# Optimization experiments

Hardware: AMD Instinct MI355X
Metric: run time of the kernel (lower is better)

## Reference

```python
import jax, jax.numpy as jnp
import numpy as np

DIM = 1024
NUM_HEADS = 16
DIM_HEAD = 64
POOL = 8  # int(sqrt(agent_num=64))
SCALE = DIM_HEAD ** -0.5


def setup_inputs() -> dict:
    key = jax.random.key(0)
    k1, k2, k3, k4 = jax.random.split(key, 4)
    inner = NUM_HEADS * DIM_HEAD
    x = jax.random.normal(k1, (4, 4096, DIM), dtype=jnp.float32)
    # qkv Linear (no bias): weight stored as (in, out) so forward is x @ Wqkv
    Wqkv = jax.random.normal(k2, (DIM, 3 * inner), dtype=jnp.float32) * (DIM ** -0.5)
    Wo = jax.random.normal(k3, (inner, DIM), dtype=jnp.float32) * (inner ** -0.5)
    bo = jax.random.normal(k4, (DIM,), dtype=jnp.float32) * 0.01
    return {"x": x, "Wqkv": Wqkv, "Wo": Wo, "bo": bo}


def reference(x, Wqkv, Wo, bo):
    b, t, _ = x.shape
    h, d = NUM_HEADS, DIM_HEAD
    qkv = x @ Wqkv                                   # [b, t, 3*h*d]
    qkv = qkv.reshape(b, t, 3, h, d)                 # split (qkv h d)
    qkv = jnp.transpose(qkv, (2, 0, 3, 1, 4))        # [3, b, h, t, d]
    q, k, v = qkv[0], qkv[1], qkv[2]
    # AdaptiveAvgPool2d((POOL, d)) on [b,h,t,d]: identity on d, mean-pool t -> POOL
    # (t divisible by POOL -> exact reshape+mean)
    agent = q.reshape(b, h, POOL, t // POOL, d).mean(axis=3)  # [b, h, P, d]
    # stage 1: agents attend over keys, aggregate values
    s1 = jnp.einsum('bhid,bhjd->bhij', agent * SCALE, k)      # [b, h, P, t]
    p1 = jax.nn.softmax(s1, axis=-1)
    v_agent = jnp.einsum('bhij,bhjd->bhid', p1, v)            # [b, h, P, d]
    # stage 2: queries attend over agent tokens
    s2 = jnp.einsum('bhid,bhjd->bhij', q * SCALE, agent)      # [b, h, t, P]
    p2 = jax.nn.softmax(s2, axis=-1)
    out = jnp.einsum('bhij,bhjd->bhid', p2, v_agent)          # [b, h, t, d]
    out = jnp.transpose(out, (0, 2, 1, 3)).reshape(b, t, h * d)
    return out @ Wo + bo
```

## Files before the change

kernel.cpp:

```cpp
#include <hip/hip_runtime.h>
#include <hip/hip_bf16.h>
#include <stdint.h>

typedef __bf16 bf16;
typedef __attribute__((ext_vector_type(8))) __bf16 bf16x8;
typedef __attribute__((ext_vector_type(2))) __bf16 bf16x2;
typedef __attribute__((ext_vector_type(4))) float f32x4;

#define NH 16
#define DH 64
#define POOL 8
#define BATCH 4
#define SEQ 4096
#define DIMV 1024
#define QKV_N (3*DIMV)
#define M_TOTAL (BATCH*SEQ)
#define SCALE_F 0.125f
#define BH (BATCH*NH)
#define QKVSZ ((size_t)BH*SEQ*DH)
#define TCH 8
#define TCL (SEQ/TCH)
#define HP 128

#define AS1(p) ((const __attribute__((address_space(1))) void*)(p))
#define AS3(p) ((__attribute__((address_space(3))) void*)(p))

__global__ void convert_x(const float* __restrict__ in, bf16* __restrict__ out) {
  size_t i = ((size_t)blockIdx.x * 256 + threadIdx.x) * 8;
  float4 f0 = *(const float4*)(in + i);
  float4 f1 = *(const float4*)(in + i + 4);
  bf16x8 o;
  o[0] = (bf16)f0.x; o[1] = (bf16)f0.y; o[2] = (bf16)f0.z; o[3] = (bf16)f0.w;
  o[4] = (bf16)f1.x; o[5] = (bf16)f1.y; o[6] = (bf16)f1.z; o[7] = (bf16)f1.w;
  *(bf16x8*)(out + i) = o;
}

__global__ void transpose_f32_bf16(const float* __restrict__ in, bf16* __restrict__ out,
                                   int R, int C) {
  __shared__ float tile[32][33];
  int c0 = blockIdx.x * 32, r0 = blockIdx.y * 32;
  int tx = threadIdx.x & 31, ty = threadIdx.x >> 5;
  for (int i = ty; i < 32; i += 8)
    tile[i][tx] = in[(size_t)(r0 + i) * C + c0 + tx];
  __syncthreads();
  for (int i = ty; i < 32; i += 8)
    out[(size_t)(c0 + i) * R + r0 + tx] = (bf16)tile[tx][i];
}

template <int MODE>
__global__ __launch_bounds__(256)
void gemm_bt(const bf16* __restrict__ A, const bf16* __restrict__ B,
             void* __restrict__ Cv, const float* __restrict__ bias,
             int M, int N, int K) {
  __shared__ bf16 As[128 * 32];
  __shared__ bf16 Bs[128 * 32];
  const int tid  = threadIdx.x;
  const int w    = tid >> 6;
  const int lane = tid & 63;
  const int m0 = blockIdx.y * 128, n0 = blockIdx.x * 128;
  const int wm = (w & 1) * 64, wn = (w >> 1) * 64;

  const bf16* Bb = (MODE == 2) ? (B + (size_t)(m0 >> 12) * N * K) : B;

  f32x4 acc[4][4] = {};

  const int g0  = w * 2;
  const int rig = lane >> 2;
  const int kcs = (lane & 3) ^ ((rig >> 1) & 3);
  const bf16* Ap0 = A + (size_t)(m0 + g0 * 16 + rig) * K + kcs * 8;
  const bf16* Ap1 = Ap0 + (size_t)16 * K;
  const bf16* Bp0 = Bb + (size_t)(n0 + g0 * 16 + rig) * K + kcs * 8;
  const bf16* Bp1 = Bp0 + (size_t)16 * K;
  bf16* AsW0 = As + g0 * 512;
  bf16* AsW1 = As + (g0 + 1) * 512;
  bf16* BsW0 = Bs + g0 * 512;
  bf16* BsW1 = Bs + (g0 + 1) * 512;

  for (int k0 = 0; k0 < K; k0 += 32) {
    __syncthreads();
    __builtin_amdgcn_global_load_lds(AS1(Ap0 + k0), AS3(AsW0), 16, 0, 0);
    __builtin_amdgcn_global_load_lds(AS1(Ap1 + k0), AS3(AsW1), 16, 0, 0);
    __builtin_amdgcn_global_load_lds(AS1(Bp0 + k0), AS3(BsW0), 16, 0, 0);
    __builtin_amdgcn_global_load_lds(AS1(Bp1 + k0), AS3(BsW1), 16, 0, 0);
    __syncthreads();

    bf16x8 a[4], b[4];
    const int C = lane >> 4;
#pragma unroll
    for (int i = 0; i < 4; ++i) {
      int ar = wm + i * 16 + (lane & 15);
      int sw = C ^ ((ar >> 1) & 3);
      a[i] = *(const bf16x8*)&As[ar * 32 + sw * 8];
    }
#pragma unroll
    for (int j = 0; j < 4; ++j) {
      int br = wn + j * 16 + (lane & 15);
      int sw = C ^ ((br >> 1) & 3);
      b[j] = *(const bf16x8*)&Bs[br * 32 + sw * 8];
    }
#pragma unroll
    for (int i = 0; i < 4; ++i)
#pragma unroll
      for (int j = 0; j < 4; ++j)
        acc[i][j] = __builtin_amdgcn_mfma_f32_16x16x32_bf16(a[i], b[j], acc[i][j], 0, 0, 0);
  }

  const int cr = (lane >> 4) * 4;
  const int cc = lane & 15;
#pragma unroll
  for (int i = 0; i < 4; ++i) {
#pragma unroll
    for (int j = 0; j < 4; ++j) {
      int rowb = m0 + wm + i * 16 + cr;
      if (MODE == 2) {
        float* Cp = (float*)Cv;
        int col = n0 + wn + j * 16 + cc;
        float bb = bias[col];
#pragma unroll
        for (int r = 0; r < 4; ++r)
          Cp[(size_t)(rowb + r) * N + col] = acc[i][j][r] + bb;
      } else {
        bf16* Cp = (bf16*)Cv;
        int nbase = n0 + wn + j * 16;
        int which = nbase >> 10;
        int hh    = (nbase >> 6) & 15;
        int dd    = (nbase & 63) + cc;
        int bb_   = rowb >> 12;
#pragma unroll
        for (int r = 0; r < 4; ++r) {
          int t = (rowb + r) & 4095;
          size_t addr = (size_t)which * QKVSZ +
                        ((size_t)(bb_ * NH + hh) * SEQ + t) * DH + dd;
          Cp[addr] = (bf16)acc[i][j][r];
        }
      }
    }
  }
}

__global__ void agent_pool(const bf16* __restrict__ q, float* __restrict__ agent) {
  int bid = blockIdx.x;
  int p = bid & 7, bh = bid >> 3;
  int d = threadIdx.x & 63, c = threadIdx.x >> 6;
  const bf16* base = q + ((size_t)bh * SEQ + p * 512) * DH + d;
  float s = 0.f;
  for (int i = c * 128; i < c * 128 + 128; ++i)
    s += (float)base[(size_t)i * DH];
  __shared__ float red[4][64];
  red[c][d] = s;
  __syncthreads();
  if (c == 0) {
    float v = (red[0][d] + red[1][d] + red[2][d] + red[3][d]) * (1.0f / 512.0f);
    agent[(size_t)(bh * POOL + p) * DH + d] = v;
  }
}

__global__ __launch_bounds__(256)
void stage1_fused(const bf16* __restrict__ k, const bf16* __restrict__ v,
                  const float* __restrict__ agent,
                  float* __restrict__ pm, float* __restrict__ pl,
                  float* __restrict__ pva) {
  const int tc = blockIdx.x, bh = blockIdx.y;
  const int tid = threadIdx.x;
  const int t0 = tc * TCL;

  __shared__ float agT[64][8];
  __shared__ float se[TCL][9];
  __shared__ float rm[4][8], rl[4][8];

  for (int i = tid; i < 512; i += 256) {
    int p = i >> 6, d = i & 63;
    agT[d][p] = agent[(size_t)bh * 512 + i] * SCALE_F;
  }
  __syncthreads();

  const bf16* kbase = k + ((size_t)bh * SEQ + t0) * DH;
  float sc[2][8] = {};
#pragma unroll
  for (int j = 0; j < 2; ++j) {
    const bf16* krow = kbase + (size_t)(j * 256 + tid) * DH;
#pragma unroll
    for (int dc = 0; dc < 8; ++dc) {
      bf16x8 k8 = *(const bf16x8*)(krow + dc * 8);
#pragma unroll
      for (int e = 0; e < 8; ++e) {
        float kv = (float)k8[e];
        int d = dc * 8 + e;
        float4 a0 = *(const float4*)&agT[d][0];
        float4 a1 = *(const float4*)&agT[d][4];
        sc[j][0] += a0.x * kv; sc[j][1] += a0.y * kv;
        sc[j][2] += a0.z * kv; sc[j][3] += a0.w * kv;
        sc[j][4] += a1.x * kv; sc[j][5] += a1.y * kv;
        sc[j][6] += a1.z * kv; sc[j][7] += a1.w * kv;
      }
    }
  }

  float mx[8];
#pragma unroll
  for (int p = 0; p < 8; ++p) mx[p] = fmaxf(sc[0][p], sc[1][p]);
#pragma unroll
  for (int o = 32; o; o >>= 1)
#pragma unroll
    for (int p = 0; p < 8; ++p) mx[p] = fmaxf(mx[p], __shfl_xor(mx[p], o));
  if ((tid & 63) == 0)
#pragma unroll
    for (int p = 0; p < 8; ++p) rm[tid >> 6][p] = mx[p];
  __syncthreads();
  float m[8];
#pragma unroll
  for (int p = 0; p < 8; ++p)
    m[p] = fmaxf(fmaxf(rm[0][p], rm[1][p]), fmaxf(rm[2][p], rm[3][p]));

  float sl[8] = {};
#pragma unroll
  for (int j = 0; j < 2; ++j) {
    int tl = j * 256 + tid;
#pragma unroll
    for (int p = 0; p < 8; ++p) {
      float e = __expf(sc[j][p] - m[p]);
      sl[p] += e;
      se[tl][p] = e;
    }
  }
#pragma unroll
  for (int o = 32; o; o >>= 1)
#pragma unroll
    for (int p = 0; p < 8; ++p) sl[p] += __shfl_xor(sl[p], o);
  if ((tid & 63) == 0)
#pragma unroll
    for (int p = 0; p < 8; ++p) rl[tid >> 6][p] = sl[p];
  __syncthreads();
  if (tid < 8) {
    float l = rl[0][tid] + rl[1][tid] + rl[2][tid] + rl[3][tid];
    pm[(size_t)(bh * TCH + tc) * 8 + tid] = m[tid];
    pl[(size_t)(bh * TCH + tc) * 8 + tid] = l;
  }

  const int p  = tid >> 5;
  const int d0 = (tid & 31) * 2;
  const bf16* vbase = v + ((size_t)bh * SEQ + t0) * DH + d0;
  float a0 = 0.f, a1 = 0.f;
#pragma unroll 8
  for (int tl = 0; tl < TCL; ++tl) {
    float wgt = se[tl][p];
    bf16x2 v2 = *(const bf16x2*)(vbase + (size_t)tl * DH);
    a0 += wgt * (float)v2[0];
    a1 += wgt * (float)v2[1];
  }
  float* o = pva + ((size_t)(bh * TCH + tc) * 8 + p) * DH + d0;
  o[0] = a0; o[1] = a1;
}

__global__ void combine_vag(const float* __restrict__ pm, const float* __restrict__ pl,
                            const float* __restrict__ pva, float* __restrict__ vag) {
  int bh = blockIdx.x;
#pragma unroll
  for (int e = threadIdx.x; e < 512; e += 256) {
    int p = e >> 6, d = e & 63;
    float M = -1e30f;
#pragma unroll
    for (int tc = 0; tc < TCH; ++tc)
      M = fmaxf(M, pm[(size_t)(bh * TCH + tc) * 8 + p]);
    float L = 0.f, acc = 0.f;
#pragma unroll
    for (int tc = 0; tc < TCH; ++tc) {
      float w = __expf(pm[(size_t)(bh * TCH + tc) * 8 + p] - M);
      L   += w * pl[(size_t)(bh * TCH + tc) * 8 + p];
      acc += w * pva[((size_t)(bh * TCH + tc) * 8 + p) * DH + d];
    }
    vag[(size_t)bh * 512 + e] = acc / L;
  }
}

__global__ void w2_build(const float* __restrict__ vag, const bf16* __restrict__ WoT,
                         bf16* __restrict__ W2T) {
  int b = blockIdx.y;
  int n = blockIdx.x * 16 + (threadIdx.x & 15);
  int h = threadIdx.x >> 4;
  __shared__ float vg[128][65];
  for (int i = threadIdx.x; i < 128 * 64; i += 256)
    vg[i >> 6][i & 63] = vag[(size_t)b * 128 * 64 + i];
  __syncthreads();
  float acc[8] = {};
  const bf16* wrow = WoT + (size_t)n * DIMV + h * 64;
#pragma unroll
  for (int dv = 0; dv < 8; ++dv) {
    bf16x8 wv = *(const bf16x8*)(wrow + dv * 8);
#pragma unroll
    for (int e = 0; e < 8; ++e) {
      float wf = (float)wv[e];
      int d = dv * 8 + e;
#pragma unroll
      for (int p = 0; p < 8; ++p) acc[p] += vg[h * 8 + p][d] * wf;
    }
  }
  bf16x8 o;
#pragma unroll
  for (int p = 0; p < 8; ++p) o[p] = (bf16)acc[p];
  *(bf16x8*)&W2T[((size_t)b * DIMV + n) * HP + h * 8] = o;
}

__global__ __launch_bounds__(256)
void p2_build(const bf16* __restrict__ q, const float* __restrict__ agent,
              bf16* __restrict__ P2) {
  const int bh = blockIdx.y;
  const int t  = blockIdx.x * 256 + threadIdx.x;
  const int tid = threadIdx.x;

  __shared__ float agT[64][8];
  for (int i = tid; i < 512; i += 256) {
    int p = i >> 6, d = i & 63;
    agT[d][p] = agent[(size_t)bh * 512 + i] * SCALE_F;
  }
  __syncthreads();

  const bf16* qrow = q + ((size_t)bh * SEQ + t) * DH;
  float sc[8] = {};
#pragma unroll
  for (int dc = 0; dc < 8; ++dc) {
    bf16x8 q8 = *(const bf16x8*)(qrow + dc * 8);
#pragma unroll
    for (int e = 0; e < 8; ++e) {
      float qv = (float)q8[e];
      int d = dc * 8 + e;
      float4 a0 = *(const float4*)&agT[d][0];
      float4 a1 = *(const float4*)&agT[d][4];
      sc[0] += a0.x * qv; sc[1] += a0.y * qv; sc[2] += a0.z * qv; sc[3] += a0.w * qv;
      sc[4] += a1.x * qv; sc[5] += a1.y * qv; sc[6] += a1.z * qv; sc[7] += a1.w * qv;
    }
  }
  float m = sc[0];
#pragma unroll
  for (int p = 1; p < 8; ++p) m = fmaxf(m, sc[p]);
  float wsum = 0.f, wgt[8];
#pragma unroll
  for (int p = 0; p < 8; ++p) { wgt[p] = __expf(sc[p] - m); wsum += wgt[p]; }
  float inv = 1.0f / wsum;
  int b = bh >> 4, h = bh & 15;
  bf16x8 o8;
#pragma unroll
  for (int p = 0; p < 8; ++p) o8[p] = (bf16)(wgt[p] * inv);
  *(bf16x8*)&P2[((size_t)(b * SEQ + t)) * HP + h * 8] = o8;
}

extern "C" void kernel_launch(void* const* d_in, const int* in_sizes, int n_in,
                              void* d_out, int out_size, void* d_ws, size_t ws_size,
                              hipStream_t stream) {
  const float* x    = (const float*)d_in[0];
  const float* Wqkv = (const float*)d_in[1];
  const float* Wo   = (const float*)d_in[2];
  const float* bo   = (const float*)d_in[3];
  float* out = (float*)d_out;

  char* ws = (char*)d_ws;
  bf16* WqkvT = (bf16*)ws;                                   ws += (size_t)QKV_N * DIMV * 2;
  bf16* WoT   = (bf16*)ws;                                   ws += (size_t)DIMV * DIMV * 2;
  bf16* qkv   = (bf16*)ws;                                   ws += 3 * QKVSZ * 2;
  char* wsu   = ws;                                          ws += (size_t)M_TOTAL * DIMV * 2;
  bf16*  xb    = (bf16*)wsu;
  bf16*  P2    = (bf16*)wsu;
  bf16*  W2T   = (bf16*)(wsu + (size_t)M_TOTAL * HP * 2);
  float* agent = (float*)ws;                                 ws += 512 * 64 * 4;
  float* pm    = (float*)ws;                                 ws += BH * TCH * 8 * 4;
  float* pl    = (float*)ws;                                 ws += BH * TCH * 8 * 4;
  float* pva   = (float*)ws;                                 ws += (size_t)BH * TCH * 8 * DH * 4;
  float* vag   = (float*)ws;                                 ws += 512 * 64 * 4;

  const bf16* qp = qkv;
  const bf16* kp = qkv + QKVSZ;
  const bf16* vp = qkv + 2 * QKVSZ;

  convert_x<<<(size_t)M_TOTAL * DIMV / (256 * 8), 256, 0, stream>>>(x, xb);
  transpose_f32_bf16<<<dim3(QKV_N / 32, DIMV / 32), 256, 0, stream>>>(Wqkv, WqkvT, DIMV, QKV_N);
  transpose_f32_bf16<<<dim3(DIMV / 32, DIMV / 32), 256, 0, stream>>>(Wo, WoT, DIMV, DIMV);

  gemm_bt<0><<<dim3(QKV_N / 128, M_TOTAL / 128), 256, 0, stream>>>(
      xb, WqkvT, (void*)qkv, nullptr, M_TOTAL, QKV_N, DIMV);

  agent_pool<<<512, 256, 0, stream>>>(qp, agent);
  p2_build<<<dim3(SEQ / 256, BH), 256, 0, stream>>>(qp, agent, P2);
  stage1_fused<<<dim3(TCH, BH), 256, 0, stream>>>(kp, vp, agent, pm, pl, pva);
  combine_vag<<<BH, 256, 0, stream>>>(pm, pl, pva, vag);
  w2_build<<<dim3(DIMV / 16, BATCH), 256, 0, stream>>>(vag, WoT, W2T);

  gemm_bt<2><<<dim3(DIMV / 128, M_TOTAL / 128), 256, 0, stream>>>(
      P2, W2T, (void*)out, bo, M_TOTAL, DIMV, HP);
}
```

Before: 363.5 us.

## Fuse agent pooling into QKV GEMM epilogue and rebalance stage1 chunking

Removes the separate agent_pool kernel by having the QKV GEMM blocks that produce Q columns reduce their accumulator tiles and atomically add column sums into a zeroed agent buffer. The division by 512 is folded into the scale constant used by downstream kernels. stage1 now uses twice as many sequence chunks, so each block holds one key row per thread. Its value aggregation loads 8-wide vectors and does a split-t reduction through shared memory. The cost is float atomics, which make the pooled sums order-nondeterministic, plus an added memset and extra reduction work in the GEMM epilogue.

```diff
diff --git a/kernel.cpp b/kernel.cpp
--- a/kernel.cpp
+++ b/kernel.cpp
@@ -16,9 +16,10 @@
 #define QKV_N (3*DIMV)
 #define M_TOTAL (BATCH*SEQ)
 #define SCALE_F 0.125f
+#define AGS_F (SCALE_F / 512.0f)
 #define BH (BATCH*NH)
 #define QKVSZ ((size_t)BH*SEQ*DH)
-#define TCH 8
+#define TCH 16
 #define TCL (SEQ/TCH)
 #define HP 128
 
@@ -51,7 +52,7 @@
 __global__ __launch_bounds__(256)
 void gemm_bt(const bf16* __restrict__ A, const bf16* __restrict__ B,
              void* __restrict__ Cv, const float* __restrict__ bias,
-             int M, int N, int K) {
+             float* __restrict__ agentSum, int M, int N, int K) {
   __shared__ bf16 As[128 * 32];
   __shared__ bf16 Bs[128 * 32];
   const int tid  = threadIdx.x;
@@ -136,28 +137,41 @@
       }
     }
   }
-}
-
-__global__ void agent_pool(const bf16* __restrict__ q, float* __restrict__ agent) {
-  int bid = blockIdx.x;
-  int p = bid & 7, bh = bid >> 3;
-  int d = threadIdx.x & 63, c = threadIdx.x >> 6;
-  const bf16* base = q + ((size_t)bh * SEQ + p * 512) * DH + d;
-  float s = 0.f;
-  for (int i = c * 128; i < c * 128 + 128; ++i)
-    s += (float)base[(size_t)i * DH];
-  __shared__ float red[4][64];
-  red[c][d] = s;
-  __syncthreads();
-  if (c == 0) {
-    float v = (red[0][d] + red[1][d] + red[2][d] + red[3][d]) * (1.0f / 512.0f);
-    agent[(size_t)(bh * POOL + p) * DH + d] = v;
+
+  if (MODE == 0 && blockIdx.x < 8) {
+    __shared__ float pool_red[4][16][4];
+    float s[4];
+#pragma unroll
+    for (int j = 0; j < 4; ++j) {
+      float t = 0.f;
+#pragma unroll
+      for (int i = 0; i < 4; ++i)
+        t += acc[i][j][0] + acc[i][j][1] + acc[i][j][2] + acc[i][j][3];
+      t += __shfl_xor(t, 16);
+      t += __shfl_xor(t, 32);
+      s[j] = t;
+    }
+    if (lane < 16) {
+#pragma unroll
+      for (int j = 0; j < 4; ++j) pool_red[w][lane][j] = s[j];
+    }
+    __syncthreads();
+    if (tid < 128) {
+      int wnH = tid >> 6, j = (tid >> 4) & 3, c2 = tid & 15;
+      float v = pool_red[wnH * 2][c2][j] + pool_red[wnH * 2 + 1][c2][j];
+      int nb  = n0 + wnH * 64 + j * 16;
+      int hh  = (nb >> 6) & 15;
+      int dd  = (nb & 63) + c2;
+      int bb_ = m0 >> 12;
+      int pp  = (m0 & 4095) >> 9;
+      atomicAdd(&agentSum[((size_t)(bb_ * NH + hh) * POOL + pp) * DH + dd], v);
+    }
   }
 }
 
 __global__ __launch_bounds__(256)
 void stage1_fused(const bf16* __restrict__ k, const bf16* __restrict__ v,
-                  const float* __restrict__ agent,
+                  const float* __restrict__ agentSum,
                   float* __restrict__ pm, float* __restrict__ pl,
                   float* __restrict__ pva) {
   const int tc = blockIdx.x, bh = blockIdx.y;
@@ -167,38 +181,33 @@
   __shared__ float agT[64][8];
   __shared__ float se[TCL][9];
   __shared__ float rm[4][8], rl[4][8];
+  __shared__ float pr[4][8][64];
 
   for (int i = tid; i < 512; i += 256) {
     int p = i >> 6, d = i & 63;
-    agT[d][p] = agent[(size_t)bh * 512 + i] * SCALE_F;
-  }
-  __syncthreads();
-
-  const bf16* kbase = k + ((size_t)bh * SEQ + t0) * DH;
-  float sc[2][8] = {};
-#pragma unroll
-  for (int j = 0; j < 2; ++j) {
-    const bf16* krow = kbase + (size_t)(j * 256 + tid) * DH;
-#pragma unroll
-    for (int dc = 0; dc < 8; ++dc) {
-      bf16x8 k8 = *(const bf16x8*)(krow + dc * 8);
-#pragma unroll
-      for (int e = 0; e < 8; ++e) {
-        float kv = (float)k8[e];
-        int d = dc * 8 + e;
-        float4 a0 = *(const float4*)&agT[d][0];
-        float4 a1 = *(const float4*)&agT[d][4];
-        sc[j][0] += a0.x * kv; sc[j][1] += a0.y * kv;
-        sc[j][2] += a0.z * kv; sc[j][3] += a0.w * kv;
-        sc[j][4] += a1.x * kv; sc[j][5] += a1.y * kv;
-        sc[j][6] += a1.z * kv; sc[j][7] += a1.w * kv;
-      }
+    agT[d][p] = agentSum[(size_t)bh * 512 + i] * AGS_F;
+  }
+  __syncthreads();
+
+  const bf16* krow = k + ((size_t)bh * SEQ + t0 + tid) * DH;
+  float sc[8] = {};
+#pragma unroll
+  for (int dc = 0; dc < 8; ++dc) {
+    bf16x8 k8 = *(const bf16x8*)(krow + dc * 8);
+#pragma unroll
+    for (int e = 0; e < 8; ++e) {
+      float kv = (float)k8[e];
+      int d = dc * 8 + e;
+      float4 a0 = *(const float4*)&agT[d][0];
+      float4 a1 = *(const float4*)&agT[d][4];
+      sc[0] += a0.x * kv; sc[1] += a0.y * kv; sc[2] += a0.z * kv; sc[3] += a0.w * kv;
+      sc[4] += a1.x * kv; sc[5] += a1.y * kv; sc[6] += a1.z * kv; sc[7] += a1.w * kv;
     }
   }
 
   float mx[8];
 #pragma unroll
-  for (int p = 0; p < 8; ++p) mx[p] = fmaxf(sc[0][p], sc[1][p]);
+  for (int p = 0; p < 8; ++p) mx[p] = sc[p];
 #pragma unroll
   for (int o = 32; o; o >>= 1)
 #pragma unroll
@@ -212,16 +221,12 @@
   for (int p = 0; p < 8; ++p)
     m[p] = fmaxf(fmaxf(rm[0][p], rm[1][p]), fmaxf(rm[2][p], rm[3][p]));
 
-  float sl[8] = {};
-#pragma unroll
-  for (int j = 0; j < 2; ++j) {
-    int tl = j * 256 + tid;
-#pragma unroll
-    for (int p = 0; p < 8; ++p) {
-      float e = __expf(sc[j][p] - m[p]);
-      sl[p] += e;
-      se[tl][p] = e;
-    }
+  float sl[8];
+#pragma unroll
+  for (int p = 0; p < 8; ++p) {
+    float e = __expf(sc[p] - m[p]);
+    se[tid][p] = e;
+    sl[p] = e;
   }
 #pragma unroll
   for (int o = 32; o; o >>= 1)
@@ -238,18 +243,26 @@
   }
 
   const int p  = tid >> 5;
-  const int d0 = (tid & 31) * 2;
-  const bf16* vbase = v + ((size_t)bh * SEQ + t0) * DH + d0;
-  float a0 = 0.f, a1 = 0.f;
-#pragma unroll 8
-  for (int tl = 0; tl < TCL; ++tl) {
+  const int dg = tid & 7;
+  const int to = (tid >> 3) & 3;
+  const bf16* vb = v + ((size_t)bh * SEQ + t0 + to) * DH + dg * 8;
+  float a8[8] = {};
+  for (int tl = to; tl < TCL; tl += 4) {
     float wgt = se[tl][p];
-    bf16x2 v2 = *(const bf16x2*)(vbase + (size_t)tl * DH);
-    a0 += wgt * (float)v2[0];
-    a1 += wgt * (float)v2[1];
-  }
-  float* o = pva + ((size_t)(bh * TCH + tc) * 8 + p) * DH + d0;
-  o[0] = a0; o[1] = a1;
+    bf16x8 v8 = *(const bf16x8*)(vb + (size_t)(tl - to) * DH);
+#pragma unroll
+    for (int e = 0; e < 8; ++e) a8[e] += wgt * (float)v8[e];
+  }
+#pragma unroll
+  for (int e = 0; e < 8; ++e) pr[to][p][dg * 8 + e] = a8[e];
+  __syncthreads();
+  if (to == 0) {
+    float* o = pva + ((size_t)(bh * TCH + tc) * 8 + p) * DH + dg * 8;
+#pragma unroll
+    for (int e = 0; e < 8; ++e)
+      o[e] = pr[0][p][dg * 8 + e] + pr[1][p][dg * 8 + e] +
+             pr[2][p][dg * 8 + e] + pr[3][p][dg * 8 + e];
+  }
 }
 
 __global__ void combine_vag(const float* __restrict__ pm, const float* __restrict__ pl,
@@ -302,7 +315,7 @@
 }
 
 __global__ __launch_bounds__(256)
-void p2_build(const bf16* __restrict__ q, const float* __restrict__ agent,
+void p2_build(const bf16* __restrict__ q, const float* __restrict__ agentSum,
               bf16* __restrict__ P2) {
   const int bh = blockIdx.y;
   const int t  = blockIdx.x * 256 + threadIdx.x;
@@ -311,7 +324,7 @@
   __shared__ float agT[64][8];
   for (int i = tid; i < 512; i += 256) {
     int p = i >> 6, d = i & 63;
-    agT[d][p] = agent[(size_t)bh * 512 + i] * SCALE_F;
+    agT[d][p] = agentSum[(size_t)bh * 512 + i] * AGS_F;
   }
   __syncthreads();
 
@@ -371,19 +384,20 @@
   const bf16* kp = qkv + QKVSZ;
   const bf16* vp = qkv + 2 * QKVSZ;
 
+  hipMemsetAsync(agent, 0, 512 * 64 * 4, stream);
+
   convert_x<<<(size_t)M_TOTAL * DIMV / (256 * 8), 256, 0, stream>>>(x, xb);
   transpose_f32_bf16<<<dim3(QKV_N / 32, DIMV / 32), 256, 0, stream>>>(Wqkv, WqkvT, DIMV, QKV_N);
   transpose_f32_bf16<<<dim3(DIMV / 32, DIMV / 32), 256, 0, stream>>>(Wo, WoT, DIMV, DIMV);
 
   gemm_bt<0><<<dim3(QKV_N / 128, M_TOTAL / 128), 256, 0, stream>>>(
-      xb, WqkvT, (void*)qkv, nullptr, M_TOTAL, QKV_N, DIMV);
-
-  agent_pool<<<512, 256, 0, stream>>>(qp, agent);
+      xb, WqkvT, (void*)qkv, nullptr, agent, M_TOTAL, QKV_N, DIMV);
+
   p2_build<<<dim3(SEQ / 256, BH), 256, 0, stream>>>(qp, agent, P2);
   stage1_fused<<<dim3(TCH, BH), 256, 0, stream>>>(kp, vp, agent, pm, pl, pva);
   combine_vag<<<BH, 256, 0, stream>>>(pm, pl, pva, vag);
   w2_build<<<dim3(DIMV / 16, BATCH), 256, 0, stream>>>(vag, WoT, W2T);
 
   gemm_bt<2><<<dim3(DIMV / 128, M_TOTAL / 128), 256, 0, stream>>>(
-      P2, W2T, (void*)out, bo, M_TOTAL, DIMV, HP);
-}
+      P2, W2T, (void*)out, bo, nullptr, M_TOTAL, DIMV, HP);
+}
```

Measured after the change: 353.8 us. 1.03x faster.
